# Kernel optimization log

Measured on AMD Instinct MI355X. Metric: run time of the kernel, lower is better.

Reference implementation:

```python
import jax, jax.numpy as jnp
import numpy as np

WINDOW_SIZE = 11
SIGMA = 1.5
CHANNEL = 1


def _gaussian_window(window_size, sigma, channel):
    x = np.arange(window_size, dtype=np.float32)
    g = np.exp(-((x - window_size // 2) ** 2) / (2.0 * sigma ** 2))
    g = g / g.sum()
    w2d = np.outer(g, g).astype(np.float32)  # (K, K)
    # torch layout: (channel, 1, K, K) for grouped (depthwise) conv
    return jnp.asarray(np.broadcast_to(w2d, (channel, 1, window_size, window_size)).copy())


def _depthwise_conv(x, window, channel):
    # x: (B, C, H, W), window: (C, 1, K, K); SAME padding, groups=C
    pad = window.shape[-1] // 2
    return jax.lax.conv_general_dilated(
        x, window,
        window_strides=(1, 1),
        padding=[(pad, pad), (pad, pad)],
        dimension_numbers=("NCHW", "OIHW", "NCHW"),
        feature_group_count=channel,
    )


def setup_inputs() -> dict:
    key = jax.random.key(0)
    k1, k2 = jax.random.split(key)
    B, C, H, W = 64, CHANNEL, 512, 512
    img1 = jax.random.uniform(k1, (B, C, H, W), dtype=jnp.float32)
    img2 = jax.random.uniform(k2, (B, C, H, W), dtype=jnp.float32)
    window = _gaussian_window(WINDOW_SIZE, SIGMA, CHANNEL)
    return {"img1": img1, "img2": img2, "window": window}


def reference(img1, img2, window):
    channel = img1.shape[1]
    C1 = 0.01 ** 2
    C2 = 0.03 ** 2
    conv = lambda t: _depthwise_conv(t, window, channel)
    mu1 = conv(img1)
    mu2 = conv(img2)
    mu1_sq = mu1 * mu1
    mu2_sq = mu2 * mu2
    mu1_mu2 = mu1 * mu2
    sigma1_sq = conv(img1 * img1) - mu1_sq
    sigma2_sq = conv(img2 * img2) - mu2_sq
    sigma12 = conv(img1 * img2) - mu1_mu2
    ssim_map = ((2.0 * mu1_mu2 + C1) * (2.0 * sigma12 + C2)) / (
        (mu1_sq + mu2_sq + C1) * (sigma1_sq + sigma2_sq + C2)
    )
    return jnp.mean(ssim_map)  # size_average=True
```

## Files before the change

### kernel.cpp

```cpp
#include <hip/hip_runtime.h>

#define IMG 512
#define BATCH 64
#define RPS 64
#define NSTEP 74
#define WPW 144

typedef float v2f __attribute__((ext_vector_type(2)));

__global__ __launch_bounds__(256, 2) void ssim_ro_kernel(
    const float* __restrict__ img1, const float* __restrict__ img2,
    const float* __restrict__ window, float* __restrict__ partials)
{
    __shared__ float S[4][2][2][WPW];
    __shared__ float wred[4];

    const int tid   = threadIdx.x;
    const int lane  = tid & 63;
    const int wv    = tid >> 6;
    const int strip = blockIdx.x;
    const int b     = blockIdx.y;
    const int r_base = strip * RPS;
    const int cbase = wv * 128;
    const int c0    = cbase + lane * 2;

    float gw[11];
    #pragma unroll
    for (int k = 0; k < 11; ++k) {
        float s = 0.f;
        #pragma unroll
        for (int j = 0; j < 11; ++j) s += window[k*11 + j];
        gw[k] = __int_as_float(__builtin_amdgcn_readfirstlane(__float_as_int(s)));
    }

    const float* P1 = img1 + (size_t)b * (IMG*IMG);
    const float* P2 = img2 + (size_t)b * (IMG*IMG);

    const bool lh = (lane < 3);
    const bool rh = (lane >= 61);
    const int  lcol = cbase - 6 + 2*lane;
    const int  rcol = cbase + 128 + 2*(lane - 61);
    const bool lok = lh && (lcol >= 0);
    const bool rok = rh && (rcol <= IMG-2);

    auto fetch = [&](int rr, v2f& o1, v2f& o2, v2f& h1_, v2f& h2_) {
        o1=(v2f){0,0}; o2=(v2f){0,0}; h1_=(v2f){0,0}; h2_=(v2f){0,0};
        if (rr >= 0 && rr < IMG) {
            const float* q1 = P1 + (size_t)rr*IMG;
            const float* q2 = P2 + (size_t)rr*IMG;
            o1 = *(const v2f*)(q1 + c0);
            o2 = *(const v2f*)(q2 + c0);
            if (lok) { h1_ = *(const v2f*)(q1 + lcol); h2_ = *(const v2f*)(q2 + lcol); }
            if (rok) { h1_ = *(const v2f*)(q1 + rcol); h2_ = *(const v2f*)(q2 + rcol); }
        }
    };
    auto store = [&](int buf, v2f o1, v2f o2, v2f h1_, v2f h2_) {
        *(v2f*)&S[wv][buf][0][6 + 2*lane] = o1 + o2;
        *(v2f*)&S[wv][buf][1][6 + 2*lane] = o1 - o2;
        if (lh) { *(v2f*)&S[wv][buf][0][2*lane] = h1_ + h2_;
                  *(v2f*)&S[wv][buf][1][2*lane] = h1_ - h2_; }
        if (rh) { *(v2f*)&S[wv][buf][0][134 + 2*(lane-61)] = h1_ + h2_;
                  *(v2f*)&S[wv][buf][1][134 + 2*(lane-61)] = h1_ - h2_; }
    };

    v2f pAo1, pAo2, pAh1, pAh2;
    v2f pBo1, pBo2, pBh1, pBh2;

    v2f ownC1, ownC2, ownN1, ownN2;

    { v2f o1,o2,e1,e2; fetch(r_base - 5, o1,o2,e1,e2); store(0, o1,o2,e1,e2);
      ownC1 = o1 + o2; ownC2 = o1 - o2; }
    fetch(r_base - 4, pAo1,pAo2,pAh1,pAh2);
    fetch(r_base - 3, pBo1,pBo2,pBh1,pBh2);

    v2f acc[11][4];
    #pragma unroll
    for (int s = 0; s < 11; ++s)
        #pragma unroll
        for (int ch = 0; ch < 4; ++ch) acc[s][ch] = (v2f){0.f, 0.f};

    v2f rsum = (v2f){0.f, 0.f};
    const float C1 = 1e-4f, C2 = 9e-4f;

    #pragma unroll 1
    for (int jj = 0; jj < 7; ++jj) {
      #pragma unroll
      for (int u = 0; u < 11; ++u) {
        if (jj < 6 || u < 8) {
          const int t = jj*11 + u;
          const int rr = r_base - 5 + t;

          const float* R1 = &S[wv][t & 1][0][0];
          const float* R2 = &S[wv][t & 1][1][0];
          v2f L1[7], L2[7];
          #pragma unroll
          for (int q = 0; q < 7; ++q) {
            if (q == 3) { L1[3] = ownC1; L2[3] = ownC2; }
            else {
              L1[q] = *(const v2f*)&R1[2*lane + 2*q];
              L2[q] = *(const v2f*)&R2[2*lane + 2*q];
            }
          }

          if ((u & 1) == 0) {
            store((t+1) & 1, pAo1,pAo2,pAh1,pAh2);
            ownN1 = pAo1 + pAo2; ownN2 = pAo1 - pAo2;
          } else {
            store((t+1) & 1, pBo1,pBo2,pBh1,pBh2);
            ownN1 = pBo1 + pBo2; ownN2 = pBo1 - pBo2;
          }

          if ((u & 1) == 0) fetch(rr + 3, pAo1,pAo2,pAh1,pAh2);
          else              fetch(rr + 3, pBo1,pBo2,pBh1,pBh2);

          __builtin_amdgcn_s_setprio(1);

          v2f hz = (v2f){0,0}, hd = (v2f){0,0};
          v2f hz2 = (v2f){0,0}, hd2 = (v2f){0,0};
          #pragma unroll
          for (int k = 0; k < 11; ++k) {
            v2f pa, pb;
            if (k & 1) {
              pa = L1[(k+1) >> 1]; pb = L2[(k+1) >> 1];
            } else {
              pa = __builtin_shufflevector(L1[k>>1], L1[(k>>1)+1], 1, 2);
              pb = __builtin_shufflevector(L2[k>>1], L2[(k>>1)+1], 1, 2);
            }
            float w = gw[k];
            hz  += w * pa;
            hd  += w * pb;
            hz2 += w * (pa * pa);
            hd2 += w * (pb * pb);
          }

          #pragma unroll
          for (int s = 0; s < 11; ++s) {
            const int k = 10 - (((s - u) % 11 + 11) % 11);
            const float w = gw[k];
            acc[s][0] += w * hz;
            acc[s][1] += w * hd;
            acc[s][2] += w * hz2;
            acc[s][3] += w * hd2;
          }

          if (t >= 10) {
            v2f vz = acc[u][0], vd = acc[u][1];
            v2f VZ2 = acc[u][2], VD2 = acc[u][3];
            v2f z2 = vz*vz, d2 = vd*vd;
            v2f A = z2 + d2, B = z2 - d2;
            v2f Ssum = VZ2 + VD2, D = VZ2 - VD2;
            v2f num = (0.5f*B + C1) * (0.5f*(D - B) + C2);
            v2f den = (0.5f*A + C1) * (0.5f*(Ssum - A) + C2);
            rsum.x += num.x * __builtin_amdgcn_rcpf(den.x);
            rsum.y += num.y * __builtin_amdgcn_rcpf(den.y);
          }
          #pragma unroll
          for (int ch = 0; ch < 4; ++ch) acc[u][ch] = (v2f){0.f, 0.f};

          __builtin_amdgcn_s_setprio(0);

          ownC1 = ownN1; ownC2 = ownN2;
        }
      }
      { v2f x;
        x=pAo1; pAo1=pBo1; pBo1=x;  x=pAo2; pAo2=pBo2; pBo2=x;
        x=pAh1; pAh1=pBh1; pBh1=x;  x=pAh2; pAh2=pBh2; pBh2=x; }
    }

    float thr_sum = rsum.x + rsum.y;

    for (int d = 32; d > 0; d >>= 1) thr_sum += __shfl_down(thr_sum, d, 64);
    if (lane == 0) wred[wv] = thr_sum;
    __syncthreads();
    if (tid == 0) {
        float s = wred[0] + wred[1] + wred[2] + wred[3];
        partials[blockIdx.y * 8 + blockIdx.x] = s;
    }
}

__global__ __launch_bounds__(256) void ssim_reduce_kernel(
    const float* __restrict__ partials, int n, float* __restrict__ out)
{
    __shared__ double wsumd[4];
    double s = 0.0;
    for (int i = threadIdx.x; i < n; i += 256) s += (double)partials[i];
    for (int d = 32; d > 0; d >>= 1) s += __shfl_down(s, d, 64);
    int wid = threadIdx.x >> 6, lane = threadIdx.x & 63;
    if (lane == 0) wsumd[wid] = s;
    __syncthreads();
    if (threadIdx.x == 0) {
        double t = wsumd[0] + wsumd[1] + wsumd[2] + wsumd[3];
        out[0] = (float)(t / ((double)BATCH * IMG * IMG));
    }
}

extern "C" void kernel_launch(void* const* d_in, const int* in_sizes, int n_in,
                              void* d_out, int out_size, void* d_ws, size_t ws_size,
                              hipStream_t stream) {
    const float* img1   = (const float*)d_in[0];
    const float* img2   = (const float*)d_in[1];
    const float* window = (const float*)d_in[2];
    float* out = (float*)d_out;
    float* partials = (float*)d_ws;

    dim3 grid(IMG / RPS, BATCH);
    ssim_ro_kernel<<<grid, dim3(256), 0, stream>>>(img1, img2, window, partials);

    int npart = (IMG / RPS) * BATCH;
    ssim_reduce_kernel<<<1, 256, 0, stream>>>(partials, npart, out);
}
```

Measured before the change: 63.31 us.

## Roll the 11-step row ring loop and load rotating weights from shared memory

Replaces the fully unrolled 11-way inner loop with a single rolled loop over all rows. A rotating counter selects the ring-buffer slot to finalize, and the per-slot vertical weights come from a precomputed LDS table instead of being folded in at compile time. Prefetch depth drops from two rows to one (single fetch set), which shrinks code size and register use. The cost is extra LDS weight loads every step, an 11-way compare/select chain to finalize the active accumulator slot, and less latency hiding on the global loads.

```diff
diff --git a/kernel.cpp b/kernel.cpp
--- a/kernel.cpp
+++ b/kernel.cpp
@@ -8,11 +8,13 @@
 
 typedef float v2f __attribute__((ext_vector_type(2)));
 
-__global__ __launch_bounds__(256, 2) void ssim_ro_kernel(
+__global__ __launch_bounds__(256, 2) void ssim_rolled_kernel(
     const float* __restrict__ img1, const float* __restrict__ img2,
     const float* __restrict__ window, float* __restrict__ partials)
 {
     __shared__ float S[4][2][2][WPW];
+    __shared__ float gwS[11];
+    __shared__ float wtab[11][12];
     __shared__ float wred[4];
 
     const int tid   = threadIdx.x;
@@ -24,14 +26,22 @@
     const int cbase = wv * 128;
     const int c0    = cbase + lane * 2;
 
+    if (tid < 11) {
+        float s = 0.f;
+        #pragma unroll
+        for (int j = 0; j < 11; ++j) s += window[tid*11 + j];
+        gwS[tid] = s;
+    }
+    __syncthreads();
+    if (tid < 132) {
+        int uu = tid / 12, ss = tid % 12;
+        wtab[uu][ss] = (ss < 11) ? gwS[10 - (((ss - uu) % 11 + 11) % 11)] : 0.f;
+    }
     float gw[11];
     #pragma unroll
-    for (int k = 0; k < 11; ++k) {
-        float s = 0.f;
-        #pragma unroll
-        for (int j = 0; j < 11; ++j) s += window[k*11 + j];
-        gw[k] = __int_as_float(__builtin_amdgcn_readfirstlane(__float_as_int(s)));
-    }
+    for (int k = 0; k < 11; ++k)
+        gw[k] = __int_as_float(__builtin_amdgcn_readfirstlane(__float_as_int(gwS[k])));
+    __syncthreads();
 
     const float* P1 = img1 + (size_t)b * (IMG*IMG);
     const float* P2 = img2 + (size_t)b * (IMG*IMG);
@@ -63,15 +73,12 @@
                   *(v2f*)&S[wv][buf][1][134 + 2*(lane-61)] = h1_ - h2_; }
     };
 
-    v2f pAo1, pAo2, pAh1, pAh2;
-    v2f pBo1, pBo2, pBh1, pBh2;
-
-    v2f ownC1, ownC2, ownN1, ownN2;
+    v2f po1, po2, ph1, ph2;
+    v2f ownC1, ownC2;
 
     { v2f o1,o2,e1,e2; fetch(r_base - 5, o1,o2,e1,e2); store(0, o1,o2,e1,e2);
       ownC1 = o1 + o2; ownC2 = o1 - o2; }
-    fetch(r_base - 4, pAo1,pAo2,pAh1,pAh2);
-    fetch(r_base - 3, pBo1,pBo2,pBh1,pBh2);
+    fetch(r_base - 4, po1,po2,ph1,ph2);
 
     v2f acc[11][4];
     #pragma unroll
@@ -82,89 +89,89 @@
     v2f rsum = (v2f){0.f, 0.f};
     const float C1 = 1e-4f, C2 = 9e-4f;
 
+    int u = 0;
     #pragma unroll 1
-    for (int jj = 0; jj < 7; ++jj) {
-      #pragma unroll
-      for (int u = 0; u < 11; ++u) {
-        if (jj < 6 || u < 8) {
-          const int t = jj*11 + u;
-          const int rr = r_base - 5 + t;
-
-          const float* R1 = &S[wv][t & 1][0][0];
-          const float* R2 = &S[wv][t & 1][1][0];
-          v2f L1[7], L2[7];
-          #pragma unroll
-          for (int q = 0; q < 7; ++q) {
+    for (int t = 0; t < NSTEP; ++t) {
+        const int rr = r_base - 5 + t;
+
+        store((t + 1) & 1, po1, po2, ph1, ph2);
+        v2f ownN1 = po1 + po2, ownN2 = po1 - po2;
+
+        const float* R1 = &S[wv][t & 1][0][0];
+        const float* R2 = &S[wv][t & 1][1][0];
+        v2f L1[7], L2[7];
+        #pragma unroll
+        for (int q = 0; q < 7; ++q) {
             if (q == 3) { L1[3] = ownC1; L2[3] = ownC2; }
             else {
-              L1[q] = *(const v2f*)&R1[2*lane + 2*q];
-              L2[q] = *(const v2f*)&R2[2*lane + 2*q];
-            }
-          }
-
-          if ((u & 1) == 0) {
-            store((t+1) & 1, pAo1,pAo2,pAh1,pAh2);
-            ownN1 = pAo1 + pAo2; ownN2 = pAo1 - pAo2;
-          } else {
-            store((t+1) & 1, pBo1,pBo2,pBh1,pBh2);
-            ownN1 = pBo1 + pBo2; ownN2 = pBo1 - pBo2;
-          }
-
-          if ((u & 1) == 0) fetch(rr + 3, pAo1,pAo2,pAh1,pAh2);
-          else              fetch(rr + 3, pBo1,pBo2,pBh1,pBh2);
-
-          __builtin_amdgcn_s_setprio(1);
-
-          v2f hz = (v2f){0,0}, hd = (v2f){0,0};
-          v2f hz2 = (v2f){0,0}, hd2 = (v2f){0,0};
-          #pragma unroll
-          for (int k = 0; k < 11; ++k) {
+                L1[q] = *(const v2f*)&R1[2*lane + 2*q];
+                L2[q] = *(const v2f*)&R2[2*lane + 2*q];
+            }
+        }
+
+        float4 w4a = *(const float4*)&wtab[u][0];
+        float4 w4b = *(const float4*)&wtab[u][4];
+        float4 w4c = *(const float4*)&wtab[u][8];
+
+        fetch(rr + 2, po1, po2, ph1, ph2);
+
+        __builtin_amdgcn_s_setprio(1);
+
+        v2f hz = (v2f){0,0}, hd = (v2f){0,0};
+        v2f hz2 = (v2f){0,0}, hd2 = (v2f){0,0};
+        #pragma unroll
+        for (int k = 0; k < 11; ++k) {
             v2f pa, pb;
             if (k & 1) {
-              pa = L1[(k+1) >> 1]; pb = L2[(k+1) >> 1];
+                pa = L1[(k+1) >> 1]; pb = L2[(k+1) >> 1];
             } else {
-              pa = __builtin_shufflevector(L1[k>>1], L1[(k>>1)+1], 1, 2);
-              pb = __builtin_shufflevector(L2[k>>1], L2[(k>>1)+1], 1, 2);
+                pa = __builtin_shufflevector(L1[k>>1], L1[(k>>1)+1], 1, 2);
+                pb = __builtin_shufflevector(L2[k>>1], L2[(k>>1)+1], 1, 2);
             }
             float w = gw[k];
             hz  += w * pa;
             hd  += w * pb;
             hz2 += w * (pa * pa);
             hd2 += w * (pb * pb);
-          }
-
-          #pragma unroll
-          for (int s = 0; s < 11; ++s) {
-            const int k = 10 - (((s - u) % 11 + 11) % 11);
-            const float w = gw[k];
-            acc[s][0] += w * hz;
-            acc[s][1] += w * hd;
-            acc[s][2] += w * hz2;
-            acc[s][3] += w * hd2;
-          }
-
-          if (t >= 10) {
-            v2f vz = acc[u][0], vd = acc[u][1];
-            v2f VZ2 = acc[u][2], VD2 = acc[u][3];
-            v2f z2 = vz*vz, d2 = vd*vd;
-            v2f A = z2 + d2, B = z2 - d2;
-            v2f Ssum = VZ2 + VD2, D = VZ2 - VD2;
-            v2f num = (0.5f*B + C1) * (0.5f*(D - B) + C2);
-            v2f den = (0.5f*A + C1) * (0.5f*(Ssum - A) + C2);
-            rsum.x += num.x * __builtin_amdgcn_rcpf(den.x);
-            rsum.y += num.y * __builtin_amdgcn_rcpf(den.y);
-          }
-          #pragma unroll
-          for (int ch = 0; ch < 4; ++ch) acc[u][ch] = (v2f){0.f, 0.f};
-
-          __builtin_amdgcn_s_setprio(0);
-
-          ownC1 = ownN1; ownC2 = ownN2;
-        }
-      }
-      { v2f x;
-        x=pAo1; pAo1=pBo1; pBo1=x;  x=pAo2; pAo2=pBo2; pBo2=x;
-        x=pAh1; pAh1=pBh1; pBh1=x;  x=pAh2; pAh2=pBh2; pBh2=x; }
+        }
+
+        {
+            const float wts[11] = { w4a.x, w4a.y, w4a.z, w4a.w,
+                                    w4b.x, w4b.y, w4b.z, w4b.w,
+                                    w4c.x, w4c.y, w4c.z };
+            #pragma unroll
+            for (int s = 0; s < 11; ++s) {
+                const float w = wts[s];
+                acc[s][0] += w * hz;
+                acc[s][1] += w * hd;
+                acc[s][2] += w * hz2;
+                acc[s][3] += w * hd2;
+            }
+        }
+
+        #pragma unroll
+        for (int s = 0; s < 11; ++s) {
+            if (s == u) {
+                if (t >= 10) {
+                    v2f vz = acc[s][0], vd = acc[s][1];
+                    v2f VZ2 = acc[s][2], VD2 = acc[s][3];
+                    v2f z2 = vz*vz, d2 = vd*vd;
+                    v2f A = z2 + d2, B = z2 - d2;
+                    v2f Ssum = VZ2 + VD2, D = VZ2 - VD2;
+                    v2f num = (0.5f*B + C1) * (0.5f*(D - B) + C2);
+                    v2f den = (0.5f*A + C1) * (0.5f*(Ssum - A) + C2);
+                    rsum.x += num.x * __builtin_amdgcn_rcpf(den.x);
+                    rsum.y += num.y * __builtin_amdgcn_rcpf(den.y);
+                }
+                #pragma unroll
+                for (int ch = 0; ch < 4; ++ch) acc[s][ch] = (v2f){0.f, 0.f};
+            }
+        }
+
+        __builtin_amdgcn_s_setprio(0);
+
+        ownC1 = ownN1; ownC2 = ownN2;
+        if (++u == 11) u = 0;
     }
 
     float thr_sum = rsum.x + rsum.y;
@@ -204,7 +211,7 @@
     float* partials = (float*)d_ws;
 
     dim3 grid(IMG / RPS, BATCH);
-    ssim_ro_kernel<<<grid, dim3(256), 0, stream>>>(img1, img2, window, partials);
+    ssim_rolled_kernel<<<grid, dim3(256), 0, stream>>>(img1, img2, window, partials);
 
     int npart = (IMG / RPS) * BATCH;
     ssim_reduce_kernel<<<1, 256, 0, stream>>>(partials, npart, out);
```

Result: slower. 75.29 us (+18.9%).
